# Kernel tuning notes

Measured on AMD Instinct MI355X. Metric: run time of the kernel, lower is better.

The kernel has to match this reference:

```python
import jax, jax.numpy as jnp
import numpy as np

S, N, D, F, E = 2048, 8, 1024, 4096, 8
STD = 0.02


def setup_inputs() -> dict:
    key = jax.random.key(0)
    ks = jax.random.split(key, 5)
    x = jax.random.normal(ks[0], (S, N, D), dtype=jnp.float32)
    Wg = jax.random.normal(ks[1], (E, D), dtype=jnp.float32) * STD
    W1 = jax.random.normal(ks[2], (E, F, D), dtype=jnp.float32) * STD
    b1 = jnp.zeros((E, F), dtype=jnp.float32)
    W2 = jax.random.normal(ks[3], (E, D, F), dtype=jnp.float32) * STD
    b2 = jnp.zeros((E, D), dtype=jnp.float32)
    return {"x": x, "Wg": Wg, "W1": W1, "b1": b1, "W2": W2, "b2": b2}


def reference(x, Wg, W1, b1, W2, b2):
    # Gate (eval mode: no gating noise). scores: [S, N, E]
    scores = jnp.einsum('snd,ed->sne', x, Wg)
    prob = jax.nn.softmax(scores, axis=-1)
    top1_idx = jnp.argmax(prob, axis=-1)                                   # [S, N] int
    top1_prob = jnp.take_along_axis(prob, top1_idx[..., None], axis=-1)[..., 0]  # [S, N]

    y = jnp.zeros_like(x)
    n_experts = Wg.shape[0]
    for e in range(n_experts):  # small fixed loop over experts
        h = jax.nn.gelu(jnp.einsum('snd,fd->snf', x, W1[e]) + b1[e], approximate=False)
        ye = jnp.einsum('snf,df->snd', h, W2[e]) + b2[e]
        mask = (top1_idx == e)[..., None]                                  # [S, N, 1]
        y = y + jnp.where(mask, ye * top1_prob[..., None], 0.0)
    return y
```

## Files before the change

kernel.cpp:

```cpp
#include <hip/hip_runtime.h>

#define S_TOK 16384
#define D_DIM 1024
#define F_DIM 4096
#define E_NUM 8

#define BM 256
#define BN 256
#define MT_MAX 72

typedef short bf16x8 __attribute__((ext_vector_type(8)));
typedef float f32x4 __attribute__((ext_vector_type(4)));
typedef unsigned short ushort_t;

static __device__ __forceinline__ unsigned short f32_bf16(float f) {
  unsigned u = __float_as_uint(f);
  return (unsigned short)((u + 0x7FFFu + ((u >> 16) & 1u)) >> 16);
}

static __device__ __forceinline__ unsigned int pack_bf16x2(float a, float b) {
  unsigned ua = __float_as_uint(a);
  unsigned ub = __float_as_uint(b);
  unsigned lo = (ua + 0x7FFFu + ((ua >> 16) & 1u)) >> 16;
  unsigned hi = (ub + 0x7FFFu + ((ub >> 16) & 1u)) & 0xFFFF0000u;
  return lo | hi;
}

static __device__ __forceinline__ uint2 cvt_f4_bf4(const float4 v) {
  uint2 r;
  r.x = pack_bf16x2(v.x, v.y);
  r.y = pack_bf16x2(v.z, v.w);
  return r;
}

static __device__ __forceinline__ void load_lds16(const void* g, void* l) {
  __builtin_amdgcn_global_load_lds(g, l, 16, 0, 0);
}

__global__ void zero_counts_kernel(int* counts) {
  if (threadIdx.x < E_NUM) counts[threadIdx.x] = 0;
}

__global__ void cast2_kernel(const float* __restrict__ w1, ushort_t* __restrict__ o1,
                             const float* __restrict__ w2, ushort_t* __restrict__ o2) {
  const int half = 16384;
  const float* src = (blockIdx.x < half) ? w1 : w2;
  ushort_t* dst = (blockIdx.x < half) ? o1 : o2;
  const int b = (blockIdx.x < half) ? blockIdx.x : (blockIdx.x - half);
  const size_t base = ((size_t)b * blockDim.x + threadIdx.x) * 8;
  const float4 v0 = *(const float4*)(src + base);
  const float4 v1 = *(const float4*)(src + base + 4);
  const uint2 a = cvt_f4_bf4(v0), c = cvt_f4_bf4(v1);
  uint4 w; w.x = a.x; w.y = a.y; w.z = c.x; w.w = c.y;
  *(uint4*)(dst + base) = w;
}

__global__ void gate_kernel(const float* __restrict__ x,
                            const float* __restrict__ Wg,
                            ushort_t* __restrict__ xbf,
                            float* __restrict__ prob,
                            int* __restrict__ counts,
                            int* __restrict__ tok_list) {
  const int wv = threadIdx.x >> 6;
  const int lane = threadIdx.x & 63;
  const int t = blockIdx.x * 4 + wv;
  const float* xr = x + (size_t)t * D_DIM;
  ushort_t* xb = xbf + (size_t)t * D_DIM;

  float acc[E_NUM];
#pragma unroll
  for (int e = 0; e < E_NUM; ++e) acc[e] = 0.0f;

#pragma unroll
  for (int i = 0; i < 4; ++i) {
    const int k = i * 256 + lane * 4;
    const float4 v = *(const float4*)(xr + k);
    *(uint2*)(xb + k) = cvt_f4_bf4(v);
#pragma unroll
    for (int e = 0; e < E_NUM; ++e) {
      const float4 w = *(const float4*)(Wg + e * D_DIM + k);
      acc[e] += v.x * w.x + v.y * w.y + v.z * w.z + v.w * w.w;
    }
  }
#pragma unroll
  for (int e = 0; e < E_NUM; ++e) {
#pragma unroll
    for (int off = 32; off > 0; off >>= 1)
      acc[e] += __shfl_xor(acc[e], off, 64);
  }
  if (lane == 0) {
    float m = acc[0]; int bi = 0;
#pragma unroll
    for (int e = 1; e < E_NUM; ++e) {
      if (acc[e] > m) { m = acc[e]; bi = e; }
    }
    float s = 0.0f;
#pragma unroll
    for (int e = 0; e < E_NUM; ++e) s += expf(acc[e] - m);
    prob[t] = 1.0f / s;
    int p = atomicAdd(&counts[bi], 1);
    tok_list[bi * S_TOK + p] = t;
  }
}

__global__ void plan_kernel(const int* __restrict__ counts, int* __restrict__ plan) {
  if (threadIdx.x == 0) {
    int t = 0;
    for (int e = 0; e < E_NUM; ++e) {
      const int nt = (counts[e] + BM - 1) / BM;
      for (int i = 0; i < nt; ++i) {
        plan[1 + t] = e;
        plan[1 + MT_MAX + t] = i * BM;
        ++t;
      }
    }
    plan[0] = t;
  }
}

template <int KDIM, int NDIM, int EPI>
__launch_bounds__(512, 2)
__global__ void ffn_kernel(const ushort_t* __restrict__ A,
                           const ushort_t* __restrict__ B,
                           const float* __restrict__ bias,
                           const float* __restrict__ prob,
                           const int* __restrict__ counts,
                           const int* __restrict__ tok_list,
                           const int* __restrict__ plan,
                           ushort_t* __restrict__ Hout,
                           float* __restrict__ out) {
  constexpr int NT = NDIM / BN;
  constexpr int NWG = NT * MT_MAX;
  constexpr int NK = KDIM / 64;
  const int ntiles = plan[0];
  const int wg = (blockIdx.x & 7) * (NWG >> 3) + (blockIdx.x >> 3);
  const int tile = wg / NT;
  if (tile >= ntiles) return;
  const int n0 = (wg % NT) * BN;
  const int e = plan[1 + tile];
  const int m0 = plan[1 + MT_MAX + tile];
  const int cnt = counts[e];

  __shared__ ushort_t Lds[2 * 4 * 8192];

  const int tid = threadIdx.x;
  const int lane = tid & 63;
  const int wid = tid >> 6;
  const int wr2 = wid >> 2;
  const int wc4 = wid & 3;
  const int l15 = lane & 15;
  const int l4  = lane >> 4;

  const int srow = tid >> 2;
  const int swel = ((tid & 3) ^ ((srow >> 1) & 3)) * 8;
  const int dstoff = wid * 512;

  const size_t ebase = (size_t)e * S_TOK;
  const int ra0 = m0 + srow, ra1 = m0 + 128 + srow;
  const int tok0 = (ra0 < cnt) ? tok_list[ebase + ra0] : 0;
  const int tok1 = (ra1 < cnt) ? tok_list[ebase + ra1] : 0;
  const ushort_t* aSrc0 = A + (size_t)tok0 * KDIM + swel;
  const ushort_t* aSrc1 = A + (size_t)tok1 * KDIM + swel;
  const ushort_t* Bebase = B + (size_t)e * NDIM * KDIM;
  const ushort_t* bSrc0 = Bebase + (size_t)(n0 + srow) * KDIM + swel;
  const ushort_t* bSrc1 = Bebase + (size_t)(n0 + 128 + srow) * KDIM + swel;

  int oA[8], oB[4];
#pragma unroll
  for (int m = 0; m < 8; ++m) {
    const int r = wr2 * 128 + m * 16 + l15;
    oA[m] = r * 32 + ((l4 ^ ((r >> 1) & 3)) * 8);
  }
#pragma unroll
  for (int n = 0; n < 4; ++n) {
    const int r = wc4 * 64 + n * 16 + l15;
    oB[n] = r * 32 + ((l4 ^ ((r >> 1) & 3)) * 8);
  }

  f32x4 acc[8][4];
#pragma unroll
  for (int i = 0; i < 8; ++i)
#pragma unroll
    for (int j = 0; j < 4; ++j)
      acc[i][j] = (f32x4){0.f, 0.f, 0.f, 0.f};

  ushort_t* cur = Lds;
  ushort_t* nxt = Lds + 32768;

  {
    load_lds16(aSrc0, cur + dstoff);
    load_lds16(aSrc1, cur + 4096 + dstoff);
    load_lds16(bSrc0, cur + 16384 + dstoff);
    load_lds16(bSrc1, cur + 16384 + 4096 + dstoff);
    load_lds16(aSrc0 + 32, cur + 8192 + dstoff);
    load_lds16(aSrc1 + 32, cur + 8192 + 4096 + dstoff);
    load_lds16(bSrc0 + 32, cur + 24576 + dstoff);
    load_lds16(bSrc1 + 32, cur + 24576 + 4096 + dstoff);
    const int t1 = (NK > 1) ? 64 : 0;
    load_lds16(aSrc0 + t1, nxt + dstoff);
    load_lds16(aSrc1 + t1, nxt + 4096 + dstoff);
    load_lds16(bSrc0 + t1, nxt + 16384 + dstoff);
    load_lds16(bSrc1 + t1, nxt + 16384 + 4096 + dstoff);
    asm volatile("s_waitcnt vmcnt(8)" ::: "memory");
    __builtin_amdgcn_s_barrier();
  }

  for (int t = 0; t < NK; ++t) {
    const int tt1 = ((t + 1 < NK) ? (t + 1) : (NK - 1)) * 64;
    const int tt2 = ((t + 2 < NK) ? (t + 2) : (NK - 1)) * 64;
    bf16x8 a[4], b[4], a2[4];

    load_lds16(aSrc0 + tt1 + 32, nxt + 8192 + dstoff);
    load_lds16(aSrc1 + tt1 + 32, nxt + 8192 + 4096 + dstoff);
#pragma unroll
    for (int i = 0; i < 4; ++i) a[i] = *(const bf16x8*)(cur + oA[i]);
#pragma unroll
    for (int n = 0; n < 4; ++n) b[n] = *(const bf16x8*)(cur + 16384 + oB[n]);
    __builtin_amdgcn_s_barrier();
    __builtin_amdgcn_s_setprio(1);
#pragma unroll
    for (int i = 0; i < 4; ++i)
#pragma unroll
      for (int n = 0; n < 4; ++n)
        acc[i][n] = __builtin_amdgcn_mfma_f32_16x16x32_bf16(a[i], b[n], acc[i][n], 0, 0, 0);
    __builtin_amdgcn_s_setprio(0);
    __builtin_amdgcn_s_barrier();

    load_lds16(bSrc0 + tt1 + 32, nxt + 24576 + dstoff);
    load_lds16(bSrc1 + tt1 + 32, nxt + 24576 + 4096 + dstoff);
#pragma unroll
    for (int i = 0; i < 4; ++i) a2[i] = *(const bf16x8*)(cur + oA[4 + i]);
    __builtin_amdgcn_s_barrier();
    __builtin_amdgcn_s_setprio(1);
#pragma unroll
    for (int i = 0; i < 4; ++i)
#pragma unroll
      for (int n = 0; n < 4; ++n)
        acc[4 + i][n] = __builtin_amdgcn_mfma_f32_16x16x32_bf16(a2[i], b[n], acc[4 + i][n], 0, 0, 0);
    __builtin_amdgcn_s_setprio(0);
    asm volatile("s_waitcnt vmcnt(8)" ::: "memory");
    __builtin_amdgcn_s_barrier();

    load_lds16(aSrc0 + tt2, cur + dstoff);
    load_lds16(aSrc1 + tt2, cur + 4096 + dstoff);
#pragma unroll
    for (int i = 0; i < 4; ++i) a[i] = *(const bf16x8*)(cur + 8192 + oA[i]);
#pragma unroll
    for (int n = 0; n < 4; ++n) b[n] = *(const bf16x8*)(cur + 24576 + oB[n]);
    __builtin_amdgcn_s_barrier();
    __builtin_amdgcn_s_setprio(1);
#pragma unroll
    for (int i = 0; i < 4; ++i)
#pragma unroll
      for (int n = 0; n < 4; ++n)
        acc[i][n] = __builtin_amdgcn_mfma_f32_16x16x32_bf16(a[i], b[n], acc[i][n], 0, 0, 0);
    __builtin_amdgcn_s_setprio(0);
    __builtin_amdgcn_s_barrier();

    load_lds16(bSrc0 + tt2, cur + 16384 + dstoff);
    load_lds16(bSrc1 + tt2, cur + 16384 + 4096 + dstoff);
#pragma unroll
    for (int i = 0; i < 4; ++i) a2[i] = *(const bf16x8*)(cur + 8192 + oA[4 + i]);
    __builtin_amdgcn_s_barrier();
    __builtin_amdgcn_s_setprio(1);
#pragma unroll
    for (int i = 0; i < 4; ++i)
#pragma unroll
      for (int n = 0; n < 4; ++n)
        acc[4 + i][n] = __builtin_amdgcn_mfma_f32_16x16x32_bf16(a2[i], b[n], acc[4 + i][n], 0, 0, 0);
    __builtin_amdgcn_s_setprio(0);
    asm volatile("s_waitcnt vmcnt(8)" ::: "memory");
    __builtin_amdgcn_s_barrier();

    ushort_t* tmp = cur; cur = nxt; nxt = tmp;
  }

  const float* be = bias + (size_t)e * NDIM;
#pragma unroll
  for (int m = 0; m < 8; ++m) {
#pragma unroll
    for (int r = 0; r < 4; ++r) {
      const int slot = m0 + wr2 * 128 + m * 16 + l4 * 4 + r;
      if (slot >= cnt) continue;
      const int tok = tok_list[ebase + slot];
      if (EPI == 0) {
        ushort_t* hrow = Hout + (size_t)tok * NDIM;
#pragma unroll
        for (int n = 0; n < 4; ++n) {
          const int col = n0 + wc4 * 64 + n * 16 + l15;
          float v = acc[m][n][r] + be[col];
          v = 0.5f * v * (1.0f + erff(v * 0.70710678118654752f));
          hrow[col] = f32_bf16(v);
        }
      } else {
        const float p = prob[tok];
        float* orow = out + (size_t)tok * NDIM;
#pragma unroll
        for (int n = 0; n < 4; ++n) {
          const int col = n0 + wc4 * 64 + n * 16 + l15;
          orow[col] = (acc[m][n][r] + be[col]) * p;
        }
      }
    }
  }
}

extern "C" void kernel_launch(void* const* d_in, const int* in_sizes, int n_in,
                              void* d_out, int out_size, void* d_ws, size_t ws_size,
                              hipStream_t stream) {
  const float* x  = (const float*)d_in[0];
  const float* Wg = (const float*)d_in[1];
  const float* W1 = (const float*)d_in[2];
  const float* b1 = (const float*)d_in[3];
  const float* W2 = (const float*)d_in[4];
  const float* b2 = (const float*)d_in[5];
  float* out = (float*)d_out;

  const size_t MB = 1ull << 20;
  char* ws = (char*)d_ws;
  int* counts      = (int*)(ws);
  int* plan        = (int*)(ws + 4096);
  float* prob      = (float*)(ws + 64 * 1024);
  int* tok_list    = (int*)(ws + 128 * 1024);
  ushort_t* xbf    = (ushort_t*)(ws + 1 * MB);
  ushort_t* W1bf   = (ushort_t*)(ws + 33 * MB);
  ushort_t* W2bf   = (ushort_t*)(ws + 97 * MB);
  ushort_t* H      = (ushort_t*)(ws + 161 * MB);

  zero_counts_kernel<<<1, 64, 0, stream>>>(counts);
  gate_kernel<<<S_TOK / 4, 256, 0, stream>>>(x, Wg, xbf, prob, counts, tok_list);
  plan_kernel<<<1, 64, 0, stream>>>(counts, plan);

  cast2_kernel<<<32768, 256, 0, stream>>>(W1, W1bf, W2, W2bf);

  ffn_kernel<D_DIM, F_DIM, 0><<<(F_DIM / BN) * MT_MAX, 512, 0, stream>>>(
      xbf, W1bf, b1, nullptr, counts, tok_list, plan, H, nullptr);

  ffn_kernel<F_DIM, D_DIM, 1><<<(D_DIM / BN) * MT_MAX, 512, 0, stream>>>(
      H, W2bf, b2, prob, counts, tok_list, plan, nullptr, out);
}
```

Baseline: 818.4 us.

## Replace hand-scheduled half-tile pipeline with simple BK=64 double-buffered loop

Replaces the four-phase interleaved schedule (split K halves, explicit s_barrier, setprio, partial vmcnt waits) with a plain double-buffered loop. Each iteration issues the whole next 64-wide K tile into the other buffer and computes both 32-wide halves from the current buffer. LDS layout changes to 64-element rows with an 8-way XOR swizzle, and loads use 8 threads per row. The change simplifies the code but drops the fine-grained load/MFMA interleaving and wave priority hints. It also relies on __syncthreads and implicit waits, which may stall on the full outstanding load queue each iteration.

New measurement: 822.0 us. No clear change (+0.4%).

```diff
diff --git a/kernel.cpp b/kernel.cpp
--- a/kernel.cpp
+++ b/kernel.cpp
@@ -7,6 +7,7 @@
 
 #define BM 256
 #define BN 256
+#define BK 64
 #define MT_MAX 72
 
 typedef short bf16x8 __attribute__((ext_vector_type(8)));
@@ -131,7 +132,7 @@
                            float* __restrict__ out) {
   constexpr int NT = NDIM / BN;
   constexpr int NWG = NT * MT_MAX;
-  constexpr int NK = KDIM / 64;
+  constexpr int NK = KDIM / BK;
   const int ntiles = plan[0];
   const int wg = (blockIdx.x & 7) * (NWG >> 3) + (blockIdx.x >> 3);
   const int tile = wg / NT;
@@ -141,7 +142,7 @@
   const int m0 = plan[1 + MT_MAX + tile];
   const int cnt = counts[e];
 
-  __shared__ ushort_t Lds[2 * 4 * 8192];
+  __shared__ ushort_t Lds[2][2][BM * BK];
 
   const int tid = threadIdx.x;
   const int lane = tid & 63;
@@ -151,30 +152,36 @@
   const int l15 = lane & 15;
   const int l4  = lane >> 4;
 
-  const int srow = tid >> 2;
-  const int swel = ((tid & 3) ^ ((srow >> 1) & 3)) * 8;
+  const int srow = tid >> 3;
+  const int sslot = ((tid & 7) ^ (srow & 7)) * 8;
   const int dstoff = wid * 512;
 
   const size_t ebase = (size_t)e * S_TOK;
-  const int ra0 = m0 + srow, ra1 = m0 + 128 + srow;
-  const int tok0 = (ra0 < cnt) ? tok_list[ebase + ra0] : 0;
-  const int tok1 = (ra1 < cnt) ? tok_list[ebase + ra1] : 0;
-  const ushort_t* aSrc0 = A + (size_t)tok0 * KDIM + swel;
-  const ushort_t* aSrc1 = A + (size_t)tok1 * KDIM + swel;
+  const ushort_t* aS[4];
+  const ushort_t* bS[4];
   const ushort_t* Bebase = B + (size_t)e * NDIM * KDIM;
-  const ushort_t* bSrc0 = Bebase + (size_t)(n0 + srow) * KDIM + swel;
-  const ushort_t* bSrc1 = Bebase + (size_t)(n0 + 128 + srow) * KDIM + swel;
-
-  int oA[8], oB[4];
+#pragma unroll
+  for (int i = 0; i < 4; ++i) {
+    const int ra = m0 + i * 64 + srow;
+    const int tok = (ra < cnt) ? tok_list[ebase + ra] : 0;
+    aS[i] = A + (size_t)tok * KDIM + sslot;
+    bS[i] = Bebase + (size_t)(n0 + i * 64 + srow) * KDIM + sslot;
+  }
+
+  int oA[8][2], oB[4][2];
 #pragma unroll
   for (int m = 0; m < 8; ++m) {
     const int r = wr2 * 128 + m * 16 + l15;
-    oA[m] = r * 32 + ((l4 ^ ((r >> 1) & 3)) * 8);
+#pragma unroll
+    for (int kk = 0; kk < 2; ++kk)
+      oA[m][kk] = r * BK + (((kk * 4 + l4) ^ (r & 7)) * 8);
   }
 #pragma unroll
   for (int n = 0; n < 4; ++n) {
     const int r = wc4 * 64 + n * 16 + l15;
-    oB[n] = r * 32 + ((l4 ^ ((r >> 1) & 3)) * 8);
+#pragma unroll
+    for (int kk = 0; kk < 2; ++kk)
+      oB[n][kk] = r * BK + (((kk * 4 + l4) ^ (r & 7)) * 8);
   }
 
   f32x4 acc[8][4];
@@ -184,95 +191,41 @@
     for (int j = 0; j < 4; ++j)
       acc[i][j] = (f32x4){0.f, 0.f, 0.f, 0.f};
 
-  ushort_t* cur = Lds;
-  ushort_t* nxt = Lds + 32768;
-
-  {
-    load_lds16(aSrc0, cur + dstoff);
-    load_lds16(aSrc1, cur + 4096 + dstoff);
-    load_lds16(bSrc0, cur + 16384 + dstoff);
-    load_lds16(bSrc1, cur + 16384 + 4096 + dstoff);
-    load_lds16(aSrc0 + 32, cur + 8192 + dstoff);
-    load_lds16(aSrc1 + 32, cur + 8192 + 4096 + dstoff);
-    load_lds16(bSrc0 + 32, cur + 24576 + dstoff);
-    load_lds16(bSrc1 + 32, cur + 24576 + 4096 + dstoff);
-    const int t1 = (NK > 1) ? 64 : 0;
-    load_lds16(aSrc0 + t1, nxt + dstoff);
-    load_lds16(aSrc1 + t1, nxt + 4096 + dstoff);
-    load_lds16(bSrc0 + t1, nxt + 16384 + dstoff);
-    load_lds16(bSrc1 + t1, nxt + 16384 + 4096 + dstoff);
-    asm volatile("s_waitcnt vmcnt(8)" ::: "memory");
-    __builtin_amdgcn_s_barrier();
-  }
-
+#pragma unroll
+  for (int i = 0; i < 4; ++i) {
+    load_lds16(aS[i], &Lds[0][0][i * 4096 + dstoff]);
+    load_lds16(bS[i], &Lds[0][1][i * 4096 + dstoff]);
+  }
+  __syncthreads();
+
+  int cb = 0;
   for (int t = 0; t < NK; ++t) {
-    const int tt1 = ((t + 1 < NK) ? (t + 1) : (NK - 1)) * 64;
-    const int tt2 = ((t + 2 < NK) ? (t + 2) : (NK - 1)) * 64;
-    bf16x8 a[4], b[4], a2[4];
-
-    load_lds16(aSrc0 + tt1 + 32, nxt + 8192 + dstoff);
-    load_lds16(aSrc1 + tt1 + 32, nxt + 8192 + 4096 + dstoff);
-#pragma unroll
-    for (int i = 0; i < 4; ++i) a[i] = *(const bf16x8*)(cur + oA[i]);
-#pragma unroll
-    for (int n = 0; n < 4; ++n) b[n] = *(const bf16x8*)(cur + 16384 + oB[n]);
-    __builtin_amdgcn_s_barrier();
-    __builtin_amdgcn_s_setprio(1);
-#pragma unroll
-    for (int i = 0; i < 4; ++i)
-#pragma unroll
-      for (int n = 0; n < 4; ++n)
-        acc[i][n] = __builtin_amdgcn_mfma_f32_16x16x32_bf16(a[i], b[n], acc[i][n], 0, 0, 0);
-    __builtin_amdgcn_s_setprio(0);
-    __builtin_amdgcn_s_barrier();
-
-    load_lds16(bSrc0 + tt1 + 32, nxt + 24576 + dstoff);
-    load_lds16(bSrc1 + tt1 + 32, nxt + 24576 + 4096 + dstoff);
-#pragma unroll
-    for (int i = 0; i < 4; ++i) a2[i] = *(const bf16x8*)(cur + oA[4 + i]);
-    __builtin_amdgcn_s_barrier();
-    __builtin_amdgcn_s_setprio(1);
-#pragma unroll
-    for (int i = 0; i < 4; ++i)
-#pragma unroll
-      for (int n = 0; n < 4; ++n)
-        acc[4 + i][n] = __builtin_amdgcn_mfma_f32_16x16x32_bf16(a2[i], b[n], acc[4 + i][n], 0, 0, 0);
-    __builtin_amdgcn_s_setprio(0);
-    asm volatile("s_waitcnt vmcnt(8)" ::: "memory");
-    __builtin_amdgcn_s_barrier();
-
-    load_lds16(aSrc0 + tt2, cur + dstoff);
-    load_lds16(aSrc1 + tt2, cur + 4096 + dstoff);
-#pragma unroll
-    for (int i = 0; i < 4; ++i) a[i] = *(const bf16x8*)(cur + 8192 + oA[i]);
-#pragma unroll
-    for (int n = 0; n < 4; ++n) b[n] = *(const bf16x8*)(cur + 24576 + oB[n]);
-    __builtin_amdgcn_s_barrier();
-    __builtin_amdgcn_s_setprio(1);
-#pragma unroll
-    for (int i = 0; i < 4; ++i)
-#pragma unroll
-      for (int n = 0; n < 4; ++n)
-        acc[i][n] = __builtin_amdgcn_mfma_f32_16x16x32_bf16(a[i], b[n], acc[i][n], 0, 0, 0);
-    __builtin_amdgcn_s_setprio(0);
-    __builtin_amdgcn_s_barrier();
-
-    load_lds16(bSrc0 + tt2, cur + 16384 + dstoff);
-    load_lds16(bSrc1 + tt2, cur + 16384 + 4096 + dstoff);
-#pragma unroll
-    for (int i = 0; i < 4; ++i) a2[i] = *(const bf16x8*)(cur + 8192 + oA[4 + i]);
-    __builtin_amdgcn_s_barrier();
-    __builtin_amdgcn_s_setprio(1);
-#pragma unroll
-    for (int i = 0; i < 4; ++i)
-#pragma unroll
-      for (int n = 0; n < 4; ++n)
-        acc[4 + i][n] = __builtin_amdgcn_mfma_f32_16x16x32_bf16(a2[i], b[n], acc[4 + i][n], 0, 0, 0);
-    __builtin_amdgcn_s_setprio(0);
-    asm volatile("s_waitcnt vmcnt(8)" ::: "memory");
-    __builtin_amdgcn_s_barrier();
-
-    ushort_t* tmp = cur; cur = nxt; nxt = tmp;
+    if (t + 1 < NK) {
+      const int k0 = (t + 1) * BK;
+      const int nb = cb ^ 1;
+#pragma unroll
+      for (int i = 0; i < 4; ++i) {
+        load_lds16(aS[i] + k0, &Lds[nb][0][i * 4096 + dstoff]);
+        load_lds16(bS[i] + k0, &Lds[nb][1][i * 4096 + dstoff]);
+      }
+    }
+
+#pragma unroll
+    for (int kk = 0; kk < 2; ++kk) {
+      bf16x8 a[8], b[4];
+#pragma unroll
+      for (int m = 0; m < 8; ++m) a[m] = *(const bf16x8*)&Lds[cb][0][oA[m][kk]];
+#pragma unroll
+      for (int n = 0; n < 4; ++n) b[n] = *(const bf16x8*)&Lds[cb][1][oB[n][kk]];
+#pragma unroll
+      for (int m = 0; m < 8; ++m)
+#pragma unroll
+        for (int n = 0; n < 4; ++n)
+          acc[m][n] = __builtin_amdgcn_mfma_f32_16x16x32_bf16(a[m], b[n], acc[m][n], 0, 0, 0);
+    }
+
+    __syncthreads();
+    cb ^= 1;
   }
 
   const float* be = bias + (size_t)e * NDIM;
```
